# Kernel tuning notes

Measured on AMD Instinct MI355X. Metric: run time of the kernel, lower is better.

## Reference

```python
import jax, jax.numpy as jnp
import numpy as np

B, T, W, L, H, TW = 2, 4096, 2048, 2048, 8, 4
HD = L // H  # head dim for block-diagonal gate projections


def setup_inputs() -> dict:
    key = jax.random.key(0)
    ks = jax.random.split(key, 16)
    inv_sqrt_w = 1.0 / np.sqrt(W)
    inv_sqrt_l = 1.0 / np.sqrt(L)
    inv_sqrt_hd = 1.0 / np.sqrt(HD)
    return {
        "x": jax.random.normal(ks[0], (B, T, W), dtype=jnp.float32),
        "segment_pos": jnp.tile(jnp.arange(T, dtype=jnp.int32), (B, 1)),
        # linear_y, linear_x: width -> lru_width
        "w_y": jax.random.normal(ks[1], (W, L), dtype=jnp.float32) * inv_sqrt_w,
        "b_y": jnp.zeros((L,), dtype=jnp.float32),
        "w_x": jax.random.normal(ks[2], (W, L), dtype=jnp.float32) * inv_sqrt_w,
        "b_x": jnp.zeros((L,), dtype=jnp.float32),
        # linear_out: lru_width -> width
        "w_out": jax.random.normal(ks[3], (L, W), dtype=jnp.float32) * inv_sqrt_l,
        "b_out": jnp.zeros((W,), dtype=jnp.float32),
        # depthwise causal temporal conv, kernel [TW, L]
        "conv_w": jax.random.normal(ks[4], (TW, L), dtype=jnp.float32) / np.sqrt(TW),
        "conv_b": jnp.zeros((L,), dtype=jnp.float32),
        # RG-LRU: a_param and two block-diagonal gate projections
        "a_param": jax.random.uniform(ks[5], (L,), dtype=jnp.float32, minval=-2.0, maxval=1.0),
        "igate_w": jax.random.normal(ks[6], (H, HD, HD), dtype=jnp.float32) * inv_sqrt_hd,
        "igate_b": jnp.zeros((H, HD), dtype=jnp.float32),
        "agate_w": jax.random.normal(ks[7], (H, HD, HD), dtype=jnp.float32) * inv_sqrt_hd,
        "agate_b": jnp.zeros((H, HD), dtype=jnp.float32),
    }


def _block_diag_linear(u, w, b):
    # u: [B,T,L] -> [B,T,H,HD] blockwise projected -> [B,T,L]
    uh = u.reshape(u.shape[0], u.shape[1], H, HD)
    y = jnp.einsum("bthd,hde->bthe", uh, w) + b
    return y.reshape(u.shape)


def _forward(x, segment_pos, w_y, b_y, w_x, b_x, w_out, b_out,
             conv_w, conv_b, a_param, igate_w, igate_b, agate_w, agate_b):
    # gate branch: linear_y + tanh-approx GELU
    y = jax.nn.gelu(jnp.einsum("btw,wl->btl", x, w_y) + b_y, approximate=True)
    # recurrent branch: linear_x
    xb = jnp.einsum("btw,wl->btl", x, w_x) + b_x
    # causal depthwise temporal conv (width TW), zero history before t=0
    x_pad = jnp.pad(xb, ((0, 0), (TW - 1, 0), (0, 0)))
    conv = conv_b + sum(conv_w[j] * x_pad[:, j:j + T] for j in range(TW))
    # RG-LRU gates
    gate_x = jax.nn.sigmoid(_block_diag_linear(conv, igate_w, igate_b))
    gate_a = jax.nn.sigmoid(_block_diag_linear(conv, agate_w, agate_b))
    log_a = -8.0 * gate_a * jax.nn.softplus(a_param)  # [B,T,L]
    a = jnp.exp(log_a)
    reset = (segment_pos == 0)[..., None]  # [B,T,1]
    multiplier = jnp.sqrt(1.0 - jnp.exp(2.0 * log_a))
    multiplier = jnp.where(reset, 1.0, multiplier)
    normed = conv * gate_x * multiplier
    a_masked = jnp.where(reset, 0.0, a)
    # diagonal linear recurrence: h_t = a_t * h_{t-1} + normed_t
    def step(h, inp):
        a_t, x_t = inp
        h = a_t * h + x_t
        return h, h
    h0 = jnp.zeros((x.shape[0], L), dtype=x.dtype)
    _, hs = jax.lax.scan(step, h0, (a_masked.transpose(1, 0, 2), normed.transpose(1, 0, 2)))
    hs = hs.transpose(1, 0, 2)  # [B,T,L]
    # elementwise gate then output projection
    return jnp.einsum("btl,lw->btw", hs * y, w_out) + b_out


def reference(x, segment_pos, w_y, b_y, w_x, b_x, w_out, b_out,
              conv_w, conv_b, a_param, igate_w, igate_b, agate_w, agate_b):
    return _forward(x, segment_pos, w_y, b_y, w_x, b_x, w_out, b_out,
                    conv_w, conv_b, a_param, igate_w, igate_b, agate_w, agate_b)
```

## Files before the change

kernel.cpp:

```cpp
#include <hip/hip_runtime.h>
#include <cstdint>
#include <math.h>

typedef _Float16 f16;
typedef f16 f16x8 __attribute__((ext_vector_type(8)));
typedef f16 f16x4 __attribute__((ext_vector_type(4)));
typedef float f32x4 __attribute__((ext_vector_type(4)));

#define BATCH 2
#define TSEQ 4096
#define WID 2048
#define LRU 2048
#define NHEAD 8
#define HDIM 256
#define MTOT (BATCH * TSEQ)
#define CT 128
#define NC (TSEQ / CT)

__device__ __forceinline__ void gl2lds16(const f16* g, f16* l) {
  __builtin_amdgcn_global_load_lds(
      (__attribute__((address_space(1))) uint32_t*)(uintptr_t)g,
      (__attribute__((address_space(3))) uint32_t*)(uint32_t)(uintptr_t)l,
      16, 0, 0);
}

__device__ __forceinline__ float fast_rcp(float x) {
  float r; asm("v_rcp_f32 %0, %1" : "=v"(r) : "v"(x)); return r;
}
__device__ __forceinline__ float fast_sigmoid(float x) {
  return fast_rcp(1.f + __expf(-x));
}
__device__ __forceinline__ float f16bits_to_f(uint32_t b) {
  return (float)__builtin_bit_cast(f16, (uint16_t)b);
}

__global__ void prep_kernel(const float* __restrict__ x, f16* __restrict__ Xh,
                            const float* __restrict__ w_y, const float* __restrict__ w_x,
                            const float* __restrict__ w_out,
                            f16* __restrict__ wyT, f16* __restrict__ wxT, f16* __restrict__ woutT,
                            const float* __restrict__ ig, const float* __restrict__ ag,
                            f16* __restrict__ igT, f16* __restrict__ agT,
                            const float* __restrict__ ap, float* __restrict__ spT) {
  __shared__ float tile[32][33];
  const int bid = blockIdx.x, t = threadIdx.x;
  if (bid < 16384) {
    int i = bid * 256 + t;
    float4 v = ((const float4*)x)[i];
    f16x4 o = { (f16)v.x, (f16)v.y, (f16)v.z, (f16)v.w };
    ((f16x4*)Xh)[i] = o;
    return;
  }
  if (bid >= 29696) {
    int i = (bid - 29696) * 256 + t;
    spT[i] = log1pf(expf(ap[i]));
    return;
  }
  const int tx = t & 31, ty = t >> 5;
  const float* ib; f16* ob; int R, C, c0, r0;
  if (bid < 28672) {
    int idx = bid - 16384;
    int z = idx >> 12, tl = idx & 4095;
    ib = z == 0 ? w_y : (z == 1 ? w_x : w_out);
    ob = z == 0 ? wyT : (z == 1 ? wxT : woutT);
    R = 2048; C = 2048;
    c0 = (tl & 63) * 32; r0 = (tl >> 6) * 32;
  } else {
    int idx = bid - 28672;
    int z = idx >> 6, tl = idx & 63;
    ib = (z < 8 ? ig : ag) + (long long)(z & 7) * HDIM * HDIM;
    ob = (z < 8 ? igT : agT) + (long long)(z & 7) * HDIM * HDIM;
    R = HDIM; C = HDIM;
    c0 = (tl & 7) * 32; r0 = (tl >> 3) * 32;
  }
#pragma unroll
  for (int i = 0; i < 32; i += 8)
    tile[ty + i][tx] = ib[(long long)(r0 + ty + i) * C + c0 + tx];
  __syncthreads();
#pragma unroll
  for (int i = 0; i < 32; i += 8)
    ob[(long long)(c0 + ty + i) * R + r0 + tx] = (f16)tile[tx][ty + i];
}

template <int MODE>
__global__ __launch_bounds__(512, 2) void gemm_256(
    const f16* __restrict__ A, const f16* __restrict__ BT,
    const float* __restrict__ bias, void* __restrict__ Cout,
    int M, int N, int K) {
  __shared__ __align__(16) f16 As[3][256 * 32];
  __shared__ __align__(16) f16 Bs[3][256 * 32];
  const int m0 = blockIdx.x * 256, n0 = blockIdx.y * 256;
  const int t = threadIdx.x;
  const int lane = t & 63, wave = t >> 6;
  const int wr = (wave >> 2) * 128;
  const int wc = (wave & 3) * 64;
  const int l15 = lane & 15, quad = lane >> 4;
  const int srow = t >> 2;
  const int sg = ((t & 3) ^ ((srow >> 1) & 3)) * 8;
  const int sl = (quad ^ ((l15 >> 1) & 3)) * 8;

  const f16* Ag = A + (long long)(m0 + srow) * K + sg;
  const f16* Bg = BT + (long long)(n0 + srow) * K + sg;
  const long long h128 = (long long)128 * K;

  auto STAGE_A = [&](int tt, int bb) {
    const f16* a = Ag + tt * 32;
    gl2lds16(a, &As[bb][t * 8]);
    gl2lds16(a + h128, &As[bb][128 * 32 + t * 8]);
  };
  auto STAGE_B = [&](int tt, int bb) {
    const f16* b = Bg + tt * 32;
    gl2lds16(b, &Bs[bb][t * 8]);
    gl2lds16(b + h128, &Bs[bb][128 * 32 + t * 8]);
  };

  f32x4 c[8][4] = {};
  const int NT = K >> 5;
  STAGE_A(0, 0); STAGE_B(0, 0); STAGE_A(1, 1); STAGE_B(1, 1);
  asm volatile("s_waitcnt vmcnt(4)" ::: "memory");
  __builtin_amdgcn_s_barrier();
  __builtin_amdgcn_sched_barrier(0);
  int bufc = 0, bufs = 2;
  for (int tt = 0; tt < NT; ++tt) {
    const f16* asrc = &As[bufc][0];
    const f16* bsrc = &Bs[bufc][0];
    f16x8 af[8], bf[4];
#pragma unroll
    for (int i = 0; i < 4; ++i)
      af[i] = *(const f16x8*)&asrc[(wr + i * 16 + l15) * 32 + sl];
#pragma unroll
    for (int j = 0; j < 4; ++j)
      bf[j] = *(const f16x8*)&bsrc[(wc + j * 16 + l15) * 32 + sl];
    if (tt + 2 < NT) STAGE_A(tt + 2, bufs);
    __builtin_amdgcn_s_barrier();
    asm volatile("s_waitcnt lgkmcnt(0)" ::: "memory");
    __builtin_amdgcn_sched_barrier(0);
    __builtin_amdgcn_s_setprio(1);
#pragma unroll
    for (int i = 0; i < 4; ++i)
#pragma unroll
      for (int j = 0; j < 4; ++j)
        c[i][j] = __builtin_amdgcn_mfma_f32_16x16x32_f16(af[i], bf[j], c[i][j], 0, 0, 0);
    __builtin_amdgcn_s_setprio(0);
    __builtin_amdgcn_s_barrier();
#pragma unroll
    for (int i = 4; i < 8; ++i)
      af[i] = *(const f16x8*)&asrc[(wr + i * 16 + l15) * 32 + sl];
    if (tt + 2 < NT) STAGE_B(tt + 2, bufs);
    if (tt + 1 < NT) {
      if (tt + 2 < NT) { asm volatile("s_waitcnt vmcnt(4)" ::: "memory"); }
      else             { asm volatile("s_waitcnt vmcnt(0)" ::: "memory"); }
    }
    __builtin_amdgcn_s_barrier();
    asm volatile("s_waitcnt lgkmcnt(0)" ::: "memory");
    __builtin_amdgcn_sched_barrier(0);
    __builtin_amdgcn_s_setprio(1);
#pragma unroll
    for (int i = 4; i < 8; ++i)
#pragma unroll
      for (int j = 0; j < 4; ++j)
        c[i][j] = __builtin_amdgcn_mfma_f32_16x16x32_f16(af[i], bf[j], c[i][j], 0, 0, 0);
    __builtin_amdgcn_s_setprio(0);
    __builtin_amdgcn_s_barrier();
    bufc = (bufc + 1 == 3) ? 0 : bufc + 1;
    bufs = (bufs + 1 == 3) ? 0 : bufs + 1;
  }
#pragma unroll
  for (int i = 0; i < 8; ++i) {
#pragma unroll
    for (int j = 0; j < 4; ++j) {
      const int col = n0 + wc + j * 16 + l15;
      const float bv = bias[col];
      const int row0 = m0 + wr + i * 16 + quad * 4;
#pragma unroll
      for (int r = 0; r < 4; ++r) {
        float v = c[i][j][r] + bv;
        long long off = (long long)(row0 + r) * N + col;
        if constexpr (MODE == 0) {
          float u = v + 0.044715f * v * v * v;
          float g = 0.5f * v * (1.f + tanhf(0.7978845608028654f * u));
          ((f16*)Cout)[off] = (f16)g;
        } else if constexpr (MODE == 1) {
          ((f16*)Cout)[off] = (f16)v;
        } else {
          ((float*)Cout)[off] = v;
        }
      }
    }
  }
}

__global__ __launch_bounds__(512, 2) void gates_fused(
    const f16* __restrict__ XBh, const float* __restrict__ cw, const float* __restrict__ cb,
    const f16* __restrict__ BiT, const f16* __restrict__ BaT,
    const float* __restrict__ ib, const float* __restrict__ ab,
    const float* __restrict__ spT, const int* __restrict__ segpos,
    uint32_t* __restrict__ AN, float* __restrict__ Ac, float* __restrict__ Hc) {
  __shared__ __align__(16) f16 As[128 * 256];
  __shared__ __align__(16) f16 Bi[256 * 32];
  __shared__ __align__(16) f16 Ba[256 * 32];
  const int m0 = blockIdx.x * 128;
  const int h = blockIdx.y;
  const int ncol0 = h * HDIM;
  const int t = threadIdx.x;
  const int lane = t & 63, wave = t >> 6;
  const int wr = (wave >> 2) * 64;
  const int wc = (wave & 3) * 64;
  const int l15 = lane & 15, quad = lane >> 4;

  const int srow = t >> 2, scol = (t & 3) * 8;
  const f16* Big = BiT + (long long)(ncol0 + srow) * HDIM + scol;
  const f16* Bag = BaT + (long long)(ncol0 + srow) * HDIM + scol;
  gl2lds16(Big, &Bi[t * 8]);
  gl2lds16(Big + (long long)128 * HDIM, &Bi[128 * 32 + t * 8]);
  gl2lds16(Bag, &Ba[t * 8]);
  gl2lds16(Bag + (long long)128 * HDIM, &Ba[128 * 32 + t * 8]);

#pragma unroll 4
  for (int it = 0; it < 8; ++it) {
    int idx = it * 512 + t;
    int r = idx >> 5, kc = idx & 31;
    int m = m0 + r, tpos = m & (TSEQ - 1);
    int colbase = ncol0 + kc * 8;
    float acc[8];
    {
      float4 c0 = *(const float4*)&cb[colbase];
      float4 c1 = *(const float4*)&cb[colbase + 4];
      acc[0] = c0.x; acc[1] = c0.y; acc[2] = c0.z; acc[3] = c0.w;
      acc[4] = c1.x; acc[5] = c1.y; acc[6] = c1.z; acc[7] = c1.w;
    }
#pragma unroll
    for (int d = 0; d < 4; ++d) {
      if (tpos >= d) {
        f16x8 xv = *(const f16x8*)&XBh[(long long)(m - d) * LRU + colbase];
        float4 w0 = *(const float4*)&cw[(3 - d) * LRU + colbase];
        float4 w1 = *(const float4*)&cw[(3 - d) * LRU + colbase + 4];
        acc[0] += w0.x * (float)xv[0]; acc[1] += w0.y * (float)xv[1];
        acc[2] += w0.z * (float)xv[2]; acc[3] += w0.w * (float)xv[3];
        acc[4] += w1.x * (float)xv[4]; acc[5] += w1.y * (float)xv[5];
        acc[6] += w1.z * (float)xv[6]; acc[7] += w1.w * (float)xv[7];
      }
    }
    f16x8 o;
#pragma unroll
    for (int k = 0; k < 8; ++k) o[k] = (f16)acc[k];
    int gs = (kc & ~7) | ((kc ^ r) & 7);
    *(f16x8*)&As[r * 256 + gs * 8] = o;
  }
  __syncthreads();

  f32x4 ci[4][4] = {};
  f32x4 ca[4][4] = {};
  for (int k0 = 0; k0 < HDIM; k0 += 32) {
    f16x8 af[4], bif[4], baf[4];
#pragma unroll
    for (int i = 0; i < 4; ++i) {
      int row = wr + i * 16 + l15;
      int g = (k0 >> 3) + quad;
      int gsw = (g & ~7) | ((g ^ row) & 7);
      af[i] = *(const f16x8*)&As[row * 256 + gsw * 8];
    }
#pragma unroll
    for (int j = 0; j < 4; ++j) {
      bif[j] = *(const f16x8*)&Bi[(wc + j * 16 + l15) * 32 + quad * 8];
      baf[j] = *(const f16x8*)&Ba[(wc + j * 16 + l15) * 32 + quad * 8];
    }
#pragma unroll
    for (int i = 0; i < 4; ++i)
#pragma unroll
      for (int j = 0; j < 4; ++j) {
        ci[i][j] = __builtin_amdgcn_mfma_f32_16x16x32_f16(af[i], bif[j], ci[i][j], 0, 0, 0);
        ca[i][j] = __builtin_amdgcn_mfma_f32_16x16x32_f16(af[i], baf[j], ca[i][j], 0, 0, 0);
      }
    __syncthreads();
    if (k0 + 32 < HDIM) {
      const f16* bi2 = Big + (k0 + 32);
      const f16* ba2 = Bag + (k0 + 32);
      gl2lds16(bi2, &Bi[t * 8]);
      gl2lds16(bi2 + (long long)128 * HDIM, &Bi[128 * 32 + t * 8]);
      gl2lds16(ba2, &Ba[t * 8]);
      gl2lds16(ba2 + (long long)128 * HDIM, &Ba[128 * 32 + t * 8]);
      __syncthreads();
    }
  }

  const int mb = m0 >> 12;
  const int cch = (m0 & (TSEQ - 1)) >> 7;
  uint32_t rsmask = 0;
#pragma unroll
  for (int i = 0; i < 4; ++i) {
    int4 sp4 = *(const int4*)&segpos[m0 + wr + i * 16 + quad * 4];
    rsmask |= (sp4.x == 0 ? 1u : 0u) << (i * 4 + 0);
    rsmask |= (sp4.y == 0 ? 1u : 0u) << (i * 4 + 1);
    rsmask |= (sp4.z == 0 ? 1u : 0u) << (i * 4 + 2);
    rsmask |= (sp4.w == 0 ? 1u : 0u) << (i * 4 + 3);
  }
  float Aw[4], hw[4];
#pragma unroll
  for (int j = 0; j < 4; ++j) {
    const int cl = wc + j * 16 + l15;
    const int col = ncol0 + cl;
    const float ibv = ib[col], abv = ab[col];
    const float sp = spT[col];
    float A4[4], h4[4];
#pragma unroll
    for (int i = 0; i < 4; ++i) {
      float Aseg = 1.f, hseg = 0.f;
#pragma unroll
      for (int r = 0; r < 4; ++r) {
        const int rowL = wr + i * 16 + quad * 4 + r;
        const int row = m0 + rowL;
        float gx = fast_sigmoid(ci[i][j][r] + ibv);
        float ga = fast_sigmoid(ca[i][j][r] + abv);
        float la = -8.f * ga * sp;
        bool rs = (rsmask >> (i * 4 + r)) & 1u;
        float a = rs ? 0.f : __expf(la);
        uint32_t afx = __float2uint_rn(a * 65536.f);
        if (afx > 65535u) afx = 65535u;
        float aq = (float)afx * (1.f / 65536.f);
        int g = cl >> 3, e = cl & 7;
        int gsw = (g & ~7) | ((g ^ rowL) & 7);
        float cv = (float)As[rowL * 256 + gsw * 8 + e];
        float mult = rs ? 1.f : sqrtf(fmaxf(1.f - aq * aq, 0.f));
        f16 nh = (f16)(cv * gx * mult);
        AN[(long long)row * LRU + col] =
            afx | ((uint32_t)__builtin_bit_cast(uint16_t, nh) << 16);
        float xq = (float)nh;
        hseg = aq * hseg + xq;
        Aseg *= aq;
      }
      A4[i] = Aseg; h4[i] = hseg;
    }
#pragma unroll
    for (int i = 0; i < 4; ++i) {
      float A = A4[i], hv = h4[i];
#pragma unroll
      for (int d = 1; d <= 2; d <<= 1) {
        int src = quad >= d ? lane - 16 * d : lane;
        float Ap = __shfl(A, src);
        float hp = __shfl(hv, src);
        if (quad >= d) { hv = A * hp + hv; A = Ap * A; }
      }
      A4[i] = __shfl(A, 48 + l15);
      h4[i] = __shfl(hv, 48 + l15);
    }
    float Awv = 1.f, hwv = 0.f;
#pragma unroll
    for (int i = 0; i < 4; ++i) { hwv = A4[i] * hwv + h4[i]; Awv *= A4[i]; }
    Aw[j] = Awv; hw[j] = hwv;
  }
  float* carry = (float*)Bi;
  __syncthreads();
  if (wr == 0 && quad == 0) {
#pragma unroll
    for (int j = 0; j < 4; ++j) {
      int cl = wc + j * 16 + l15;
      carry[cl * 2] = Aw[j]; carry[cl * 2 + 1] = hw[j];
    }
  }
  __syncthreads();
  if (wr == 64 && quad == 0) {
#pragma unroll
    for (int j = 0; j < 4; ++j) {
      int cl = wc + j * 16 + l15;
      float At = carry[cl * 2], ht = carry[cl * 2 + 1];
      float A = At * Aw[j];
      float hv = Aw[j] * ht + hw[j];
      int o = (mb * NC + cch) * LRU + ncol0 + cl;
      Ac[o] = A; Hc[o] = hv;
    }
  }
}

__global__ void scan23_kernel(const uint32_t* __restrict__ AN,
                              const float* __restrict__ Ac, const float* __restrict__ Hc,
                              const f16* __restrict__ Yh, f16* __restrict__ G) {
  int l = blockIdx.x * 256 + threadIdx.x;
  int c = blockIdx.y, b = blockIdx.z;
  float hv = 0.f;
  for (int cc = 0; cc < c; ++cc) {
    int o = (b * NC + cc) * LRU + l;
    hv = Ac[o] * hv + Hc[o];
  }
  long long base = ((long long)b * TSEQ + (long long)c * CT) * LRU + l;
#pragma unroll 4
  for (int s = 0; s < CT; ++s) {
    long long o = base + (long long)s * LRU;
    uint32_t p = AN[o];
    float a = (float)(p & 0xFFFFu) * (1.f / 65536.f);
    float x = f16bits_to_f(p >> 16);
    hv = a * hv + x;
    G[o] = (f16)(hv * (float)Yh[o]);
  }
}

extern "C" void kernel_launch(void* const* d_in, const int* in_sizes, int n_in,
                              void* d_out, int out_size, void* d_ws, size_t ws_size,
                              hipStream_t stream) {
  (void)in_sizes; (void)n_in; (void)out_size; (void)ws_size;
  const float* x          = (const float*)d_in[0];
  const int*   segment_pos= (const int*)d_in[1];
  const float* w_y        = (const float*)d_in[2];
  const float* b_y        = (const float*)d_in[3];
  const float* w_x        = (const float*)d_in[4];
  const float* b_x        = (const float*)d_in[5];
  const float* w_out      = (const float*)d_in[6];
  const float* b_out      = (const float*)d_in[7];
  const float* conv_w     = (const float*)d_in[8];
  const float* conv_b     = (const float*)d_in[9];
  const float* a_param    = (const float*)d_in[10];
  const float* igate_w    = (const float*)d_in[11];
  const float* igate_b    = (const float*)d_in[12];
  const float* agate_w    = (const float*)d_in[13];
  const float* agate_b    = (const float*)d_in[14];
  float* out = (float*)d_out;

  char* base = (char*)d_ws;
  size_t off = 0;
  auto alloc = [&](size_t nbytes) -> void* {
    void* p = base + off;
    off = (off + nbytes + 255) & ~(size_t)255;
    return p;
  };
  f16*     Xh    = (f16*)alloc((size_t)MTOT * LRU * 2);
  f16*     Yh    = (f16*)alloc((size_t)MTOT * LRU * 2);
  f16*     XBh   = (f16*)alloc((size_t)MTOT * LRU * 2);
  uint32_t* AN   = (uint32_t*)alloc((size_t)MTOT * LRU * 4);
  f16*     wyT   = (f16*)alloc((size_t)WID * LRU * 2);
  f16*     wxT   = (f16*)alloc((size_t)WID * LRU * 2);
  f16*     woutT = (f16*)alloc((size_t)LRU * WID * 2);
  f16*     igwT  = (f16*)alloc((size_t)NHEAD * HDIM * HDIM * 2);
  f16*     agwT  = (f16*)alloc((size_t)NHEAD * HDIM * HDIM * 2);
  float*   Ac    = (float*)alloc((size_t)BATCH * NC * LRU * 4);
  float*   Hc    = (float*)alloc((size_t)BATCH * NC * LRU * 4);
  float*   spT   = (float*)alloc((size_t)LRU * 4);
  f16*     G     = Xh;

  prep_kernel<<<29704, 256, 0, stream>>>(x, Xh, w_y, w_x, w_out, wyT, wxT, woutT,
                                         igate_w, agate_w, igwT, agwT, a_param, spT);
  gemm_256<0><<<dim3(MTOT / 256, LRU / 256), 512, 0, stream>>>(
      Xh, wyT, b_y, Yh, MTOT, LRU, WID);
  gemm_256<1><<<dim3(MTOT / 256, LRU / 256), 512, 0, stream>>>(
      Xh, wxT, b_x, XBh, MTOT, LRU, WID);
  gates_fused<<<dim3(MTOT / 128, NHEAD), 512, 0, stream>>>(
      XBh, conv_w, conv_b, igwT, agwT, igate_b, agate_b, spT, segment_pos, AN, Ac, Hc);
  scan23_kernel<<<dim3(LRU / 256, NC, BATCH), 256, 0, stream>>>(AN, Ac, Hc, Yh, G);
  gemm_256<2><<<dim3(MTOT / 256, WID / 256), 512, 0, stream>>>(
      G, woutT, b_out, out, MTOT, WID, LRU);
}
```

Measured before the change: 519.1 us.

## Restructure GEMM main loop to 64-wide K tiles with double-buffered half-tile staging

The 256x256 GEMM now stages K in 64-wide slices, each split into two 128-row halves, with double buffering in place of the previous triple buffer of 32-wide slices. The swizzle is widened to 8 chunks. Each iteration is split into eight MFMA phases that interleave A-fragment reads, async global-to-LDS loads and barriers. The aim is fewer loop iterations and better overlap of loads with MFMA work. In exchange there are many more barriers per iteration, and with only two buffers the wait-count bookkeeping is fragile.

```diff
diff --git a/kernel.cpp b/kernel.cpp
--- a/kernel.cpp
+++ b/kernel.cpp
@@ -81,89 +81,105 @@
     ob[(long long)(c0 + ty + i) * R + r0 + tx] = (f16)tile[tx][ty + i];
 }
 
+#define BAR() __builtin_amdgcn_s_barrier()
+#define LGKM0() do { asm volatile("s_waitcnt lgkmcnt(0)" ::: "memory"); \
+                     __builtin_amdgcn_sched_barrier(0); } while (0)
+#define VM4() asm volatile("s_waitcnt vmcnt(4)" ::: "memory")
+#define VM0() asm volatile("s_waitcnt vmcnt(0)" ::: "memory")
+
 template <int MODE>
 __global__ __launch_bounds__(512, 2) void gemm_256(
     const f16* __restrict__ A, const f16* __restrict__ BT,
     const float* __restrict__ bias, void* __restrict__ Cout,
     int M, int N, int K) {
-  __shared__ __align__(16) f16 As[3][256 * 32];
-  __shared__ __align__(16) f16 Bs[3][256 * 32];
+  __shared__ __align__(16) f16 As[2][2][128 * 64];
+  __shared__ __align__(16) f16 Bs[2][2][128 * 64];
   const int m0 = blockIdx.x * 256, n0 = blockIdx.y * 256;
   const int t = threadIdx.x;
-  const int lane = t & 63, wave = t >> 6;
+  const int lane = t & 63;
+  const int wave = t >> 6;
   const int wr = (wave >> 2) * 128;
   const int wc = (wave & 3) * 64;
   const int l15 = lane & 15, quad = lane >> 4;
-  const int srow = t >> 2;
-  const int sg = ((t & 3) ^ ((srow >> 1) & 3)) * 8;
-  const int sl = (quad ^ ((l15 >> 1) & 3)) * 8;
-
-  const f16* Ag = A + (long long)(m0 + srow) * K + sg;
-  const f16* Bg = BT + (long long)(n0 + srow) * K + sg;
-  const long long h128 = (long long)128 * K;
-
-  auto STAGE_A = [&](int tt, int bb) {
-    const f16* a = Ag + tt * 32;
-    gl2lds16(a, &As[bb][t * 8]);
-    gl2lds16(a + h128, &As[bb][128 * 32 + t * 8]);
-  };
-  auto STAGE_B = [&](int tt, int bb) {
-    const f16* b = Bg + tt * 32;
-    gl2lds16(b, &Bs[bb][t * 8]);
-    gl2lds16(b + h128, &Bs[bb][128 * 32 + t * 8]);
-  };
+  const int ah = wave >> 2;
+  const int bh = wc >> 7;
+  const int brow0 = wc & 127;
+
+  const int srow = t >> 3;
+  const int sgg = ((t & 7) ^ (srow & 7)) * 8;
+  const f16* Agb = A + (long long)(m0 + srow) * K + sgg;
+  const f16* Bgb = BT + (long long)(n0 + srow) * K + sgg;
+  const long long r64 = (long long)64 * K;
+  const long long r128 = (long long)128 * K;
+
+#define STAGE_OP(gb, db, kt)                                          \
+  { const f16* s_ = (gb) + (long long)(kt) * 64;                      \
+    gl2lds16(s_,              &(db)[0][t * 8]);                       \
+    gl2lds16(s_ + r64,        &(db)[0][4096 + t * 8]);                \
+    gl2lds16(s_ + r128,       &(db)[1][t * 8]);                       \
+    gl2lds16(s_ + r128 + r64, &(db)[1][4096 + t * 8]); }
+
+#define LDA(dst, buf, mf, kh)                                         \
+  { const int r_ = (mf) * 16 + l15;                                   \
+    const int s_ = ((((kh) * 4 + quad) ^ (l15 & 7)) * 8);             \
+    dst = *(const f16x8*)&As[buf][ah][r_ * 64 + s_]; }
+#define LDB(dst, buf, nf, kh)                                         \
+  { const int r_ = brow0 + (nf) * 16 + l15;                           \
+    const int s_ = ((((kh) * 4 + quad) ^ (l15 & 7)) * 8);             \
+    dst = *(const f16x8*)&Bs[buf][bh][r_ * 64 + s_]; }
+
+#define READ_B(buf)                                                   \
+  _Pragma("unroll") for (int j = 0; j < 4; ++j) {                     \
+    LDB(bf[j][0], buf, j, 0); LDB(bf[j][1], buf, j, 1); }
+#define READ_A(buf, q)                                                \
+  LDA(af[0][0], buf, 2 * (q), 0);     LDA(af[0][1], buf, 2 * (q), 1); \
+  LDA(af[1][0], buf, 2 * (q) + 1, 0); LDA(af[1][1], buf, 2 * (q) + 1, 1);
+#define MFMA16(q)                                                     \
+  __builtin_amdgcn_s_setprio(1);                                      \
+  _Pragma("unroll") for (int kh = 0; kh < 2; ++kh)                    \
+  _Pragma("unroll") for (int r = 0; r < 2; ++r)                       \
+  _Pragma("unroll") for (int j = 0; j < 4; ++j)                       \
+    c[2 * (q) + r][j] = __builtin_amdgcn_mfma_f32_16x16x32_f16(       \
+        af[r][kh], bf[j][kh], c[2 * (q) + r][j], 0, 0, 0);            \
+  __builtin_amdgcn_s_setprio(0);
 
   f32x4 c[8][4] = {};
-  const int NT = K >> 5;
-  STAGE_A(0, 0); STAGE_B(0, 0); STAGE_A(1, 1); STAGE_B(1, 1);
-  asm volatile("s_waitcnt vmcnt(4)" ::: "memory");
-  __builtin_amdgcn_s_barrier();
+  f16x8 af[2][2], bf[4][2];
+  const int NIT = K >> 7;
+
+  STAGE_OP(Bgb, Bs[0], 0);
+  STAGE_OP(Agb, As[0], 0);
+  STAGE_OP(Bgb, Bs[1], 1);
+  VM4();
+  BAR();
   __builtin_amdgcn_sched_barrier(0);
-  int bufc = 0, bufs = 2;
-  for (int tt = 0; tt < NT; ++tt) {
-    const f16* asrc = &As[bufc][0];
-    const f16* bsrc = &Bs[bufc][0];
-    f16x8 af[8], bf[4];
-#pragma unroll
-    for (int i = 0; i < 4; ++i)
-      af[i] = *(const f16x8*)&asrc[(wr + i * 16 + l15) * 32 + sl];
-#pragma unroll
-    for (int j = 0; j < 4; ++j)
-      bf[j] = *(const f16x8*)&bsrc[(wc + j * 16 + l15) * 32 + sl];
-    if (tt + 2 < NT) STAGE_A(tt + 2, bufs);
-    __builtin_amdgcn_s_barrier();
-    asm volatile("s_waitcnt lgkmcnt(0)" ::: "memory");
-    __builtin_amdgcn_sched_barrier(0);
-    __builtin_amdgcn_s_setprio(1);
-#pragma unroll
-    for (int i = 0; i < 4; ++i)
-#pragma unroll
-      for (int j = 0; j < 4; ++j)
-        c[i][j] = __builtin_amdgcn_mfma_f32_16x16x32_f16(af[i], bf[j], c[i][j], 0, 0, 0);
-    __builtin_amdgcn_s_setprio(0);
-    __builtin_amdgcn_s_barrier();
-#pragma unroll
-    for (int i = 4; i < 8; ++i)
-      af[i] = *(const f16x8*)&asrc[(wr + i * 16 + l15) * 32 + sl];
-    if (tt + 2 < NT) STAGE_B(tt + 2, bufs);
-    if (tt + 1 < NT) {
-      if (tt + 2 < NT) { asm volatile("s_waitcnt vmcnt(4)" ::: "memory"); }
-      else             { asm volatile("s_waitcnt vmcnt(0)" ::: "memory"); }
-    }
-    __builtin_amdgcn_s_barrier();
-    asm volatile("s_waitcnt lgkmcnt(0)" ::: "memory");
-    __builtin_amdgcn_sched_barrier(0);
-    __builtin_amdgcn_s_setprio(1);
-#pragma unroll
-    for (int i = 4; i < 8; ++i)
-#pragma unroll
-      for (int j = 0; j < 4; ++j)
-        c[i][j] = __builtin_amdgcn_mfma_f32_16x16x32_f16(af[i], bf[j], c[i][j], 0, 0, 0);
-    __builtin_amdgcn_s_setprio(0);
-    __builtin_amdgcn_s_barrier();
-    bufc = (bufc + 1 == 3) ? 0 : bufc + 1;
-    bufs = (bufs + 1 == 3) ? 0 : bufs + 1;
-  }
+
+  for (int i = 0; i < NIT; ++i) {
+    const bool more = (i + 1 < NIT);
+    READ_B(0); READ_A(0, 0);
+    STAGE_OP(Agb, As[1], 2 * i + 1);
+    BAR(); LGKM0(); MFMA16(0); BAR();
+    READ_A(0, 1);
+    if (more) STAGE_OP(Bgb, Bs[0], 2 * i + 2);
+    BAR(); LGKM0(); MFMA16(1); BAR();
+    READ_A(0, 2);
+    BAR(); LGKM0(); MFMA16(2); BAR();
+    READ_A(0, 3);
+    if (more) { VM4(); } else { VM0(); }
+    BAR(); LGKM0(); MFMA16(3); BAR();
+    READ_B(1); READ_A(1, 0);
+    if (more) STAGE_OP(Agb, As[0], 2 * i + 2);
+    BAR(); LGKM0(); MFMA16(0); BAR();
+    READ_A(1, 1);
+    if (more) STAGE_OP(Bgb, Bs[1], 2 * i + 3);
+    BAR(); LGKM0(); MFMA16(1); BAR();
+    READ_A(1, 2);
+    BAR(); LGKM0(); MFMA16(2); BAR();
+    READ_A(1, 3);
+    if (more) VM4();
+    BAR(); LGKM0(); MFMA16(3); BAR();
+  }
+
 #pragma unroll
   for (int i = 0; i < 8; ++i) {
 #pragma unroll
@@ -187,6 +203,12 @@
       }
     }
   }
+#undef STAGE_OP
+#undef LDA
+#undef LDB
+#undef READ_B
+#undef READ_A
+#undef MFMA16
 }
 
 __global__ __launch_bounds__(512, 2) void gates_fused(
```

Result: faster. 487.1 us (-6.2%).

## Replace triple-buffered 256x256 GEMM with simple 128x128 single-buffer GEMM

Applied to the files above, without the earlier changes.

Swaps the 256x256 tile, 512-thread, triple-buffered pipelined GEMM for a 128x128 tile, 256-thread kernel with a 64-wide K step, a single LDS buffer and plain __syncthreads between load and compute. The goal is more blocks, higher occupancy and less LDS per block. In exchange it gives up overlap of global-to-LDS loads with MFMA work and reuses each loaded element across fewer outputs, so global traffic per FLOP rises.

```diff
diff --git a/kernel.cpp b/kernel.cpp
--- a/kernel.cpp
+++ b/kernel.cpp
@@ -82,90 +82,56 @@
 }
 
 template <int MODE>
-__global__ __launch_bounds__(512, 2) void gemm_256(
+__global__ __launch_bounds__(256, 3) void gemm_128(
     const f16* __restrict__ A, const f16* __restrict__ BT,
     const float* __restrict__ bias, void* __restrict__ Cout,
     int M, int N, int K) {
-  __shared__ __align__(16) f16 As[3][256 * 32];
-  __shared__ __align__(16) f16 Bs[3][256 * 32];
-  const int m0 = blockIdx.x * 256, n0 = blockIdx.y * 256;
+  __shared__ __align__(16) f16 As[128 * 64];
+  __shared__ __align__(16) f16 Bs[128 * 64];
+  const int m0 = blockIdx.x * 128, n0 = blockIdx.y * 128;
   const int t = threadIdx.x;
   const int lane = t & 63, wave = t >> 6;
-  const int wr = (wave >> 2) * 128;
-  const int wc = (wave & 3) * 64;
+  const int wr = (wave >> 1) * 64, wc = (wave & 1) * 64;
   const int l15 = lane & 15, quad = lane >> 4;
-  const int srow = t >> 2;
-  const int sg = ((t & 3) ^ ((srow >> 1) & 3)) * 8;
-  const int sl = (quad ^ ((l15 >> 1) & 3)) * 8;
+  const int srow = t >> 3;
+  const int sg = ((t & 7) ^ (srow & 7)) * 8;
 
   const f16* Ag = A + (long long)(m0 + srow) * K + sg;
   const f16* Bg = BT + (long long)(n0 + srow) * K + sg;
-  const long long h128 = (long long)128 * K;
-
-  auto STAGE_A = [&](int tt, int bb) {
-    const f16* a = Ag + tt * 32;
-    gl2lds16(a, &As[bb][t * 8]);
-    gl2lds16(a + h128, &As[bb][128 * 32 + t * 8]);
-  };
-  auto STAGE_B = [&](int tt, int bb) {
-    const f16* b = Bg + tt * 32;
-    gl2lds16(b, &Bs[bb][t * 8]);
-    gl2lds16(b + h128, &Bs[bb][128 * 32 + t * 8]);
-  };
-
-  f32x4 c[8][4] = {};
-  const int NT = K >> 5;
-  STAGE_A(0, 0); STAGE_B(0, 0); STAGE_A(1, 1); STAGE_B(1, 1);
-  asm volatile("s_waitcnt vmcnt(4)" ::: "memory");
-  __builtin_amdgcn_s_barrier();
-  __builtin_amdgcn_sched_barrier(0);
-  int bufc = 0, bufs = 2;
-  for (int tt = 0; tt < NT; ++tt) {
-    const f16* asrc = &As[bufc][0];
-    const f16* bsrc = &Bs[bufc][0];
-    f16x8 af[8], bf[4];
-#pragma unroll
-    for (int i = 0; i < 4; ++i)
-      af[i] = *(const f16x8*)&asrc[(wr + i * 16 + l15) * 32 + sl];
-#pragma unroll
-    for (int j = 0; j < 4; ++j)
-      bf[j] = *(const f16x8*)&bsrc[(wc + j * 16 + l15) * 32 + sl];
-    if (tt + 2 < NT) STAGE_A(tt + 2, bufs);
-    __builtin_amdgcn_s_barrier();
-    asm volatile("s_waitcnt lgkmcnt(0)" ::: "memory");
-    __builtin_amdgcn_sched_barrier(0);
-    __builtin_amdgcn_s_setprio(1);
-#pragma unroll
-    for (int i = 0; i < 4; ++i)
-#pragma unroll
-      for (int j = 0; j < 4; ++j)
-        c[i][j] = __builtin_amdgcn_mfma_f32_16x16x32_f16(af[i], bf[j], c[i][j], 0, 0, 0);
-    __builtin_amdgcn_s_setprio(0);
-    __builtin_amdgcn_s_barrier();
-#pragma unroll
-    for (int i = 4; i < 8; ++i)
-      af[i] = *(const f16x8*)&asrc[(wr + i * 16 + l15) * 32 + sl];
-    if (tt + 2 < NT) STAGE_B(tt + 2, bufs);
-    if (tt + 1 < NT) {
-      if (tt + 2 < NT) { asm volatile("s_waitcnt vmcnt(4)" ::: "memory"); }
-      else             { asm volatile("s_waitcnt vmcnt(0)" ::: "memory"); }
-    }
-    __builtin_amdgcn_s_barrier();
-    asm volatile("s_waitcnt lgkmcnt(0)" ::: "memory");
-    __builtin_amdgcn_sched_barrier(0);
-    __builtin_amdgcn_s_setprio(1);
-#pragma unroll
-    for (int i = 4; i < 8; ++i)
-#pragma unroll
-      for (int j = 0; j < 4; ++j)
-        c[i][j] = __builtin_amdgcn_mfma_f32_16x16x32_f16(af[i], bf[j], c[i][j], 0, 0, 0);
-    __builtin_amdgcn_s_setprio(0);
-    __builtin_amdgcn_s_barrier();
-    bufc = (bufc + 1 == 3) ? 0 : bufc + 1;
-    bufs = (bufs + 1 == 3) ? 0 : bufs + 1;
-  }
-#pragma unroll
-  for (int i = 0; i < 8; ++i) {
+  const long long r32 = (long long)32 * K;
+
+  f32x4 c[4][4] = {};
+  const int NT = K >> 6;
+  for (int kt = 0; kt < NT; ++kt) {
+    const f16* a = Ag + kt * 64;
+    const f16* b = Bg + kt * 64;
+#pragma unroll
+    for (int cc = 0; cc < 4; ++cc) {
+      gl2lds16(a + cc * r32, &As[cc * 2048 + t * 8]);
+      gl2lds16(b + cc * r32, &Bs[cc * 2048 + t * 8]);
+    }
+    __syncthreads();
+    f16x8 af[4][2], bf[4][2];
+#pragma unroll
+    for (int f = 0; f < 4; ++f) {
+#pragma unroll
+      for (int kh = 0; kh < 2; ++kh) {
+        const int sa = ((kh * 4 + quad) ^ (l15 & 7)) * 8;
+        af[f][kh] = *(const f16x8*)&As[(wr + f * 16 + l15) * 64 + sa];
+        bf[f][kh] = *(const f16x8*)&Bs[(wc + f * 16 + l15) * 64 + sa];
+      }
+    }
+#pragma unroll
+    for (int kh = 0; kh < 2; ++kh)
+#pragma unroll
+      for (int i = 0; i < 4; ++i)
+#pragma unroll
+        for (int j = 0; j < 4; ++j)
+          c[i][j] = __builtin_amdgcn_mfma_f32_16x16x32_f16(af[i][kh], bf[j][kh], c[i][j], 0, 0, 0);
+    __syncthreads();
+  }
+#pragma unroll
+  for (int i = 0; i < 4; ++i) {
 #pragma unroll
     for (int j = 0; j < 4; ++j) {
       const int col = n0 + wc + j * 16 + l15;
@@ -437,13 +403,13 @@
 
   prep_kernel<<<29704, 256, 0, stream>>>(x, Xh, w_y, w_x, w_out, wyT, wxT, woutT,
                                          igate_w, agate_w, igwT, agwT, a_param, spT);
-  gemm_256<0><<<dim3(MTOT / 256, LRU / 256), 512, 0, stream>>>(
+  gemm_128<0><<<dim3(MTOT / 128, LRU / 128), 256, 0, stream>>>(
       Xh, wyT, b_y, Yh, MTOT, LRU, WID);
-  gemm_256<1><<<dim3(MTOT / 256, LRU / 256), 512, 0, stream>>>(
+  gemm_128<1><<<dim3(MTOT / 128, LRU / 128), 256, 0, stream>>>(
       Xh, wxT, b_x, XBh, MTOT, LRU, WID);
   gates_fused<<<dim3(MTOT / 128, NHEAD), 512, 0, stream>>>(
       XBh, conv_w, conv_b, igwT, agwT, igate_b, agate_b, spT, segment_pos, AN, Ac, Hc);
   scan23_kernel<<<dim3(LRU / 256, NC, BATCH), 256, 0, stream>>>(AN, Ac, Hc, Yh, G);
-  gemm_256<2><<<dim3(MTOT / 256, WID / 256), 512, 0, stream>>>(
+  gemm_128<2><<<dim3(MTOT / 128, WID / 128), 256, 0, stream>>>(
       G, woutT, b_out, out, MTOT, WID, LRU);
 }
```

Result: faster. 501.5 us (-3.4%).
